# Optimization experiments

Hardware: AMD Instinct MI355X
Metric: run time of the kernel (lower is better)

## Reference

```python
import jax, jax.numpy as jnp
import numpy as np

B, S, D = 8, 4096, 512
BLOCK, LEFT, RIGHT = 64, 1, 1
FF = 2048
EPS = 1e-6


def setup_inputs() -> dict:
    key = jax.random.key(0)
    ks = jax.random.split(key, 16)
    sd = 1.0 / np.sqrt(D)
    sf = 1.0 / np.sqrt(FF)
    return {
        "x": jax.random.normal(ks[0], (B, S, D), jnp.float32),
        "Wq": jax.random.normal(ks[1], (D, D), jnp.float32) * sd,
        "bq": jnp.zeros((D,), jnp.float32),
        "Wk": jax.random.normal(ks[2], (D, D), jnp.float32) * sd,
        "bk": jnp.zeros((D,), jnp.float32),
        "Wv": jax.random.normal(ks[3], (D, D), jnp.float32) * sd,
        "bv": jnp.zeros((D,), jnp.float32),
        "W1": jax.random.normal(ks[4], (D, FF), jnp.float32) * sd,
        "b1": jnp.zeros((FF,), jnp.float32),
        "W2": jax.random.normal(ks[5], (FF, D), jnp.float32) * sf,
        "b2": jnp.zeros((D,), jnp.float32),
        "g1": jnp.ones((D,), jnp.float32),
        "be1": jnp.zeros((D,), jnp.float32),
        "g2": jnp.ones((D,), jnp.float32),
        "be2": jnp.zeros((D,), jnp.float32),
    }


def layernorm(x, g, b):
    m = jnp.mean(x, axis=-1, keepdims=True)
    v = jnp.mean(jnp.square(x - m), axis=-1, keepdims=True)
    return g * (x - m) * jax.lax.rsqrt(v + EPS) + b


def local_attention(x, Wq, bq, Wk, bk, Wv, bv):
    Bsz, Sl, Dm = x.shape
    nb = Sl // BLOCK          # number of blocks
    nw = LEFT + RIGHT + 1     # window (in blocks)
    q = (x @ Wq + bq).reshape(Bsz, nb, BLOCK, Dm)
    k = (x @ Wk + bk).reshape(Bsz, nb, BLOCK, Dm)
    v = (x @ Wv + bv).reshape(Bsz, nb, BLOCK, Dm)
    # pad block axis so every query block has LEFT/RIGHT neighbor blocks
    kp = jnp.pad(k, ((0, 0), (LEFT, RIGHT), (0, 0), (0, 0)))
    vp = jnp.pad(v, ((0, 0), (LEFT, RIGHT), (0, 0), (0, 0)))
    # gather windows: (B, nb, nw*BLOCK, D)
    k_win = jnp.stack([kp[:, j:j + nb] for j in range(nw)], axis=2).reshape(Bsz, nb, nw * BLOCK, Dm)
    v_win = jnp.stack([vp[:, j:j + nb] for j in range(nw)], axis=2).reshape(Bsz, nb, nw * BLOCK, Dm)
    # mask out-of-range (padded) blocks at sequence edges
    blk = jnp.arange(nb)[:, None] + jnp.arange(nw)[None, :] - LEFT  # (nb, nw)
    mask = ((blk >= 0) & (blk < nb))
    mask = jnp.repeat(mask, BLOCK, axis=1)  # (nb, nw*BLOCK)
    scores = jnp.einsum('bnqd,bnkd->bnqk', q, k_win) / jnp.sqrt(jnp.float32(Dm))
    scores = jnp.where(mask[None, :, None, :], scores, jnp.float32(-1e9))
    attn = jax.nn.softmax(scores, axis=-1)
    out = jnp.einsum('bnqk,bnkd->bnqd', attn, v_win)
    return out.reshape(Bsz, Sl, Dm)


def reference(x, Wq, bq, Wk, bk, Wv, bv, W1, b1, W2, b2, g1, be1, g2, be2):
    # inference mode: dropout is identity
    a = local_attention(x, Wq, bq, Wk, bk, Wv, bv)
    out1 = layernorm(x + a, g1, be1)
    ffn = jnp.maximum(out1 @ W1 + b1, 0.0) @ W2 + b2
    return layernorm(out1 + ffn, g2, be2)
```

## Files before the change

kernel.cpp:

```cpp
#include <hip/hip_runtime.h>


typedef __bf16 bf16;
typedef __bf16 bf16x8 __attribute__((ext_vector_type(8)));
typedef float  f32x4  __attribute__((ext_vector_type(4)));

#define DEV __device__ __forceinline__

#define BAR()  do { asm volatile("" ::: "memory"); __builtin_amdgcn_s_barrier(); asm volatile("" ::: "memory"); } while (0)
#define WAITV(n) asm volatile("s_waitcnt vmcnt(" #n ")" ::: "memory")
#define WAITL()  asm volatile("s_waitcnt lgkmcnt(0)" ::: "memory")

DEV void gload_lds16(const void* g, void* lds) {
  __builtin_amdgcn_global_load_lds(
      (const __attribute__((address_space(1))) void*)g,
      (__attribute__((address_space(3))) void*)lds, 16, 0, 0);
}

__global__ __launch_bounds__(256) void cast_to_bf16(const float* __restrict__ in,
                                                    bf16* __restrict__ out, int n8) {
  int i = blockIdx.x * 256 + threadIdx.x;
  if (i >= n8) return;
  float4 a0 = ((const float4*)in)[i * 2];
  float4 a1 = ((const float4*)in)[i * 2 + 1];
  bf16x8 o;
  o[0] = (bf16)a0.x; o[1] = (bf16)a0.y; o[2] = (bf16)a0.z; o[3] = (bf16)a0.w;
  o[4] = (bf16)a1.x; o[5] = (bf16)a1.y; o[6] = (bf16)a1.z; o[7] = (bf16)a1.w;
  ((bf16x8*)out)[i] = o;
}

__global__ __launch_bounds__(256) void transpose_cast(const float* __restrict__ W,
                                                      bf16* __restrict__ Wt, int K, int N) {
  __shared__ bf16 tile[64][66];
  const int n0 = blockIdx.x * 64, k0 = blockIdx.y * 64;
  const int t = threadIdx.x;
#pragma unroll
  for (int it = 0; it < 16; ++it) {
    int c = it * 256 + t;
    int kr = c >> 6, nc = c & 63;
    tile[nc][kr] = (bf16)W[(size_t)(k0 + kr) * N + n0 + nc];
  }
  __syncthreads();
#pragma unroll
  for (int it = 0; it < 2; ++it) {
    int c = it * 256 + t;
    int nr = c >> 3, kg = (c & 7) * 8;
    bf16x8 v;
#pragma unroll
    for (int e = 0; e < 8; ++e) v[e] = tile[nr][kg + e];
    *(bf16x8*)(Wt + (size_t)(n0 + nr) * K + k0 + kg) = v;
  }
}

__global__ __launch_bounds__(256) void concat_bias(const float* __restrict__ bq,
                                                   const float* __restrict__ bk,
                                                   const float* __restrict__ bv,
                                                   float* __restrict__ o) {
  int i = blockIdx.x * 256 + threadIdx.x;
  if (i < 512) o[i] = bq[i];
  else if (i < 1024) o[i] = bk[i - 512];
  else if (i < 1536) o[i] = bv[i - 1024];
}

template <int RELU, int F32OUT>
__global__ __launch_bounds__(512, 1)
void gemm256(const bf16* __restrict__ A, const bf16* __restrict__ Bt,
             const float* __restrict__ bias, void* __restrict__ Cout,
             int M, int N, int K) {
  __shared__ bf16x8 lds8[6144];
  char* const LB = (char*)lds8;
  const int tid = threadIdx.x;
  const int w = tid >> 6, l = tid & 63;
  const int lr = l & 15, lg = l >> 4;
  const int wm = w >> 2, wn = w & 3;

  const int nwg = gridDim.x * gridDim.y;
  const int bid = blockIdx.y * gridDim.x + blockIdx.x;
  const int cpx = nwg >> 3;
  const int swzb = (bid & 7) * cpx + (bid >> 3);
  const int m0 = (swzb & 127) * 256;
  const int n0 = (swzb >> 7) * 256;

  const int NT = K >> 5;

  const int srow = tid >> 2;
  const int scol = (((tid & 3) ^ (srow & 3)) << 3);
  const int swz = ((lg ^ (lr & 3)) << 4);

  f32x4 acc[8][4];
#pragma unroll
  for (int i = 0; i < 8; ++i)
#pragma unroll
    for (int j = 0; j < 4; ++j) acc[i][j] = f32x4{0.f, 0.f, 0.f, 0.f};

  auto stageA = [&](int t) {
    const bf16* g = A + (size_t)(m0 + srow) * K + t * 32 + scol;
    char* d = LB + (t % 3) * 32768 + tid * 16;
    gload_lds16(g, d);
    gload_lds16(g + (size_t)128 * K, d + 8192);
  };
  auto stageB = [&](int t) {
    const bf16* g = Bt + (size_t)(n0 + srow) * K + t * 32 + scol;
    char* d = LB + (t % 3) * 32768 + 16384 + tid * 16;
    gload_lds16(g, d);
    gload_lds16(g + (size_t)128 * K, d + 8192);
  };

  stageA(0); stageB(0);
  stageA(1); stageB(1);
  WAITV(4);
  BAR();

  for (int t = 0; t < NT; ++t) {
    const char* base = LB + (t % 3) * 32768;
    const char* pA = base + (wm << 13) + lr * 64 + swz;
    const char* pB = base + 16384 + (wn << 12) + lr * 64 + swz;
    if (t + 2 < NT) { stageA(t + 2); stageB(t + 2); }
    bf16x8 a0 = *(const bf16x8*)(pA);
    bf16x8 a1 = *(const bf16x8*)(pA + 1024);
    bf16x8 a2 = *(const bf16x8*)(pA + 2048);
    bf16x8 a3 = *(const bf16x8*)(pA + 3072);
    bf16x8 a4 = *(const bf16x8*)(pA + 4096);
    bf16x8 a5 = *(const bf16x8*)(pA + 5120);
    bf16x8 a6 = *(const bf16x8*)(pA + 6144);
    bf16x8 a7 = *(const bf16x8*)(pA + 7168);
    bf16x8 b0 = *(const bf16x8*)(pB);
    bf16x8 b1 = *(const bf16x8*)(pB + 1024);
    bf16x8 b2 = *(const bf16x8*)(pB + 2048);
    bf16x8 b3 = *(const bf16x8*)(pB + 3072);
    WAITL();
    __builtin_amdgcn_s_setprio(1);
    acc[0][0] = __builtin_amdgcn_mfma_f32_16x16x32_bf16(a0, b0, acc[0][0], 0, 0, 0);
    acc[0][1] = __builtin_amdgcn_mfma_f32_16x16x32_bf16(a0, b1, acc[0][1], 0, 0, 0);
    acc[0][2] = __builtin_amdgcn_mfma_f32_16x16x32_bf16(a0, b2, acc[0][2], 0, 0, 0);
    acc[0][3] = __builtin_amdgcn_mfma_f32_16x16x32_bf16(a0, b3, acc[0][3], 0, 0, 0);
    acc[1][0] = __builtin_amdgcn_mfma_f32_16x16x32_bf16(a1, b0, acc[1][0], 0, 0, 0);
    acc[1][1] = __builtin_amdgcn_mfma_f32_16x16x32_bf16(a1, b1, acc[1][1], 0, 0, 0);
    acc[1][2] = __builtin_amdgcn_mfma_f32_16x16x32_bf16(a1, b2, acc[1][2], 0, 0, 0);
    acc[1][3] = __builtin_amdgcn_mfma_f32_16x16x32_bf16(a1, b3, acc[1][3], 0, 0, 0);
    acc[2][0] = __builtin_amdgcn_mfma_f32_16x16x32_bf16(a2, b0, acc[2][0], 0, 0, 0);
    acc[2][1] = __builtin_amdgcn_mfma_f32_16x16x32_bf16(a2, b1, acc[2][1], 0, 0, 0);
    acc[2][2] = __builtin_amdgcn_mfma_f32_16x16x32_bf16(a2, b2, acc[2][2], 0, 0, 0);
    acc[2][3] = __builtin_amdgcn_mfma_f32_16x16x32_bf16(a2, b3, acc[2][3], 0, 0, 0);
    acc[3][0] = __builtin_amdgcn_mfma_f32_16x16x32_bf16(a3, b0, acc[3][0], 0, 0, 0);
    acc[3][1] = __builtin_amdgcn_mfma_f32_16x16x32_bf16(a3, b1, acc[3][1], 0, 0, 0);
    acc[3][2] = __builtin_amdgcn_mfma_f32_16x16x32_bf16(a3, b2, acc[3][2], 0, 0, 0);
    acc[3][3] = __builtin_amdgcn_mfma_f32_16x16x32_bf16(a3, b3, acc[3][3], 0, 0, 0);
    acc[4][0] = __builtin_amdgcn_mfma_f32_16x16x32_bf16(a4, b0, acc[4][0], 0, 0, 0);
    acc[4][1] = __builtin_amdgcn_mfma_f32_16x16x32_bf16(a4, b1, acc[4][1], 0, 0, 0);
    acc[4][2] = __builtin_amdgcn_mfma_f32_16x16x32_bf16(a4, b2, acc[4][2], 0, 0, 0);
    acc[4][3] = __builtin_amdgcn_mfma_f32_16x16x32_bf16(a4, b3, acc[4][3], 0, 0, 0);
    acc[5][0] = __builtin_amdgcn_mfma_f32_16x16x32_bf16(a5, b0, acc[5][0], 0, 0, 0);
    acc[5][1] = __builtin_amdgcn_mfma_f32_16x16x32_bf16(a5, b1, acc[5][1], 0, 0, 0);
    acc[5][2] = __builtin_amdgcn_mfma_f32_16x16x32_bf16(a5, b2, acc[5][2], 0, 0, 0);
    acc[5][3] = __builtin_amdgcn_mfma_f32_16x16x32_bf16(a5, b3, acc[5][3], 0, 0, 0);
    acc[6][0] = __builtin_amdgcn_mfma_f32_16x16x32_bf16(a6, b0, acc[6][0], 0, 0, 0);
    acc[6][1] = __builtin_amdgcn_mfma_f32_16x16x32_bf16(a6, b1, acc[6][1], 0, 0, 0);
    acc[6][2] = __builtin_amdgcn_mfma_f32_16x16x32_bf16(a6, b2, acc[6][2], 0, 0, 0);
    acc[6][3] = __builtin_amdgcn_mfma_f32_16x16x32_bf16(a6, b3, acc[6][3], 0, 0, 0);
    acc[7][0] = __builtin_amdgcn_mfma_f32_16x16x32_bf16(a7, b0, acc[7][0], 0, 0, 0);
    acc[7][1] = __builtin_amdgcn_mfma_f32_16x16x32_bf16(a7, b1, acc[7][1], 0, 0, 0);
    acc[7][2] = __builtin_amdgcn_mfma_f32_16x16x32_bf16(a7, b2, acc[7][2], 0, 0, 0);
    acc[7][3] = __builtin_amdgcn_mfma_f32_16x16x32_bf16(a7, b3, acc[7][3], 0, 0, 0);
    __builtin_amdgcn_s_setprio(0);
    if (t + 2 < NT) { WAITV(4); }
    else if (t + 2 == NT) { WAITV(0); }
    BAR();
  }

  if (!F32OUT) {
    bf16* cl = (bf16*)LB;
    bf16* Cb = (bf16*)Cout;
#pragma unroll
    for (int half = 0; half < 2; ++half) {
      if (wm == half) {
#pragma unroll
        for (int n = 0; n < 4; ++n) {
          const int col = (wn << 6) + (n << 4) + lr;
          const float bv = bias[n0 + col];
#pragma unroll
          for (int m = 0; m < 8; ++m)
#pragma unroll
            for (int rg = 0; rg < 4; ++rg) {
              const int row = (m << 4) + (lg << 2) + rg;
              float v = acc[m][n][rg] + bv;
              if (RELU) v = fmaxf(v, 0.f);
              cl[row * 256 + col] = (bf16)v;
            }
        }
      }
      __syncthreads();
#pragma unroll
      for (int it = 0; it < 8; ++it) {
        const int idx = it * 512 + tid;
        const int r = idx >> 5, ch = idx & 31;
        *(bf16x8*)(Cb + (size_t)(m0 + half * 128 + r) * N + n0 + (ch << 3)) =
            *(const bf16x8*)(cl + r * 256 + (ch << 3));
      }
      __syncthreads();
    }
  } else {
    float* Cf = (float*)Cout;
#pragma unroll
    for (int n = 0; n < 4; ++n) {
      const int col = n0 + (wn << 6) + (n << 4) + lr;
      const float bv = bias[col];
#pragma unroll
      for (int m = 0; m < 8; ++m)
#pragma unroll
        for (int rg = 0; rg < 4; ++rg) {
          const int row = m0 + (wm << 7) + (m << 4) + (lg << 2) + rg;
          float v = acc[m][n][rg] + bv;
          if (RELU) v = fmaxf(v, 0.f);
          Cf[(size_t)row * N + col] = v;
        }
    }
  }
}

__global__ __launch_bounds__(256) void transpose_v(const bf16* __restrict__ qkv,
                                                   bf16* __restrict__ vt) {
  __shared__ bf16 tile[64][66];
  const int s0 = blockIdx.x * 64, d0 = blockIdx.y * 64, b = blockIdx.z;
  const int t = threadIdx.x;
#pragma unroll
  for (int it = 0; it < 2; ++it) {
    int c = it * 256 + t;
    int r = c >> 3, g = (c & 7) * 8;
    bf16x8 v = *(const bf16x8*)(qkv + ((size_t)b * 4096 + s0 + r) * 1536 + 1024 + d0 + g);
#pragma unroll
    for (int e = 0; e < 8; ++e) tile[g + e][r] = v[e];
  }
  __syncthreads();
#pragma unroll
  for (int it = 0; it < 2; ++it) {
    int c = it * 256 + t;
    int dr = c >> 3, sg = (c & 7) * 8;
    bf16x8 v;
#pragma unroll
    for (int e = 0; e < 8; ++e) v[e] = tile[dr][sg + e];
    *(bf16x8*)(vt + ((size_t)b * 512 + d0 + dr) * 4096 + s0 + sg) = v;
  }
}

__global__ __launch_bounds__(512, 4)
void attn_local(const bf16* __restrict__ qkv, const bf16* __restrict__ vt,
                bf16* __restrict__ aout) {
  __shared__ bf16 P[4][16][200];
  __shared__ float xmx[4][2][16];
  __shared__ float xsm[4][2][16];
  const int qb = blockIdx.x, b = blockIdx.y;
  const int t = threadIdx.x, w = t >> 6, l = t & 63;
  const int rg = w & 3, h = w >> 2;
  const int lr = l & 15, lg = l >> 4;

  bool val[6];
#pragma unroll
  for (int n = 0; n < 6; ++n) {
    int gn = 6 * h + n;
    val[n] = ((unsigned)(qb - 1 + (gn >> 2)) < 64u);
  }

  const size_t qrow = (size_t)b * 4096 + qb * 64 + rg * 16;
  const bf16* qp = qkv + (qrow + lr) * 1536 + lg * 8;
  const bf16* kbase = qkv + ((long)b * 4096 + (long)(qb - 1) * 64) * 1536 + 512;

  f32x4 S[6];
#pragma unroll
  for (int n = 0; n < 6; ++n) S[n] = f32x4{0.f, 0.f, 0.f, 0.f};

  for (int kk = 0; kk < 16; ++kk) {
    bf16x8 aq = *(const bf16x8*)(qp + kk * 32);
#pragma unroll
    for (int n = 0; n < 6; ++n) {
      if (!val[n]) continue;
      const int gn = 6 * h + n;
      bf16x8 bk = *(const bf16x8*)(kbase + (size_t)(gn * 16 + lr) * 1536 + kk * 32 + lg * 8);
      S[n] = __builtin_amdgcn_mfma_f32_16x16x32_bf16(aq, bk, S[n], 0, 0, 0);
    }
  }

  const float scale = 0.044194173824159216f;
  float mx[4] = {-3e38f, -3e38f, -3e38f, -3e38f};
#pragma unroll
  for (int n = 0; n < 6; ++n) {
    if (!val[n]) continue;
#pragma unroll
    for (int i = 0; i < 4; ++i) mx[i] = fmaxf(mx[i], S[n][i]);
  }
#pragma unroll
  for (int i = 0; i < 4; ++i) {
    mx[i] = fmaxf(mx[i], __shfl_xor(mx[i], 1));
    mx[i] = fmaxf(mx[i], __shfl_xor(mx[i], 2));
    mx[i] = fmaxf(mx[i], __shfl_xor(mx[i], 4));
    mx[i] = fmaxf(mx[i], __shfl_xor(mx[i], 8));
  }
  if (lr == 0) {
#pragma unroll
    for (int i = 0; i < 4; ++i) xmx[rg][h][lg * 4 + i] = mx[i];
  }
  __syncthreads();
  float m4[4];
#pragma unroll
  for (int i = 0; i < 4; ++i) m4[i] = fmaxf(mx[i], xmx[rg][h ^ 1][lg * 4 + i]);

  float sm[4] = {0.f, 0.f, 0.f, 0.f};
#pragma unroll
  for (int n = 0; n < 6; ++n) {
    if (!val[n]) continue;
#pragma unroll
    for (int i = 0; i < 4; ++i) {
      float p = __expf((S[n][i] - m4[i]) * scale);
      S[n][i] = p;
      sm[i] += p;
    }
  }
#pragma unroll
  for (int i = 0; i < 4; ++i) {
    sm[i] += __shfl_xor(sm[i], 1);
    sm[i] += __shfl_xor(sm[i], 2);
    sm[i] += __shfl_xor(sm[i], 4);
    sm[i] += __shfl_xor(sm[i], 8);
  }
  if (lr == 0) {
#pragma unroll
    for (int i = 0; i < 4; ++i) xsm[rg][h][lg * 4 + i] = sm[i];
  }
  __syncthreads();
  float rinv[4];
#pragma unroll
  for (int i = 0; i < 4; ++i) rinv[i] = 1.f / (sm[i] + xsm[rg][h ^ 1][lg * 4 + i]);

#pragma unroll
  for (int n = 0; n < 6; ++n) {
    const int gn = 6 * h + n;
#pragma unroll
    for (int i = 0; i < 4; ++i)
      P[rg][lg * 4 + i][gn * 16 + lr] = val[n] ? (bf16)(S[n][i] * rinv[i]) : (bf16)0.f;
  }
  __syncthreads();

  f32x4 O[4][4];
#pragma unroll
  for (int rt = 0; rt < 4; ++rt)
#pragma unroll
    for (int dt = 0; dt < 4; ++dt) O[rt][dt] = f32x4{0.f, 0.f, 0.f, 0.f};

  const bf16* vtb = vt + ((long)b * 512 + w * 64) * 4096 + (long)(qb - 1) * 64;
#pragma unroll
  for (int ks = 0; ks < 6; ++ks) {
    if ((unsigned)(qb - 1 + (ks >> 1)) >= 64u) continue;
    bf16x8 vf[4];
#pragma unroll
    for (int dt = 0; dt < 4; ++dt)
      vf[dt] = *(const bf16x8*)(vtb + (size_t)(dt * 16 + lr) * 4096 + ks * 32 + lg * 8);
#pragma unroll
    for (int rt = 0; rt < 4; ++rt) {
      bf16x8 pa = *(const bf16x8*)&P[rt][lr][ks * 32 + lg * 8];
#pragma unroll
      for (int dt = 0; dt < 4; ++dt)
        O[rt][dt] = __builtin_amdgcn_mfma_f32_16x16x32_bf16(pa, vf[dt], O[rt][dt], 0, 0, 0);
    }
  }

  const size_t orow = (size_t)b * 4096 + qb * 64;
#pragma unroll
  for (int rt = 0; rt < 4; ++rt)
#pragma unroll
    for (int dt = 0; dt < 4; ++dt)
#pragma unroll
      for (int i = 0; i < 4; ++i)
        aout[(orow + rt * 16 + lg * 4 + i) * 512 + w * 64 + dt * 16 + lr] =
            (bf16)O[rt][dt][i];
}

__global__ __launch_bounds__(256) void ln_res1(const float* __restrict__ x,
                                               const bf16* __restrict__ a,
                                               const float* __restrict__ g,
                                               const float* __restrict__ be,
                                               bf16* __restrict__ out) {
  const int t = threadIdx.x, w = t >> 6, l = t & 63;
  const size_t row = (size_t)blockIdx.x * 4 + w;
  const float* xp = x + row * 512 + l * 8;
  float4 x0 = ((const float4*)xp)[0];
  float4 x1 = ((const float4*)xp)[1];
  bf16x8 av = *(const bf16x8*)(a + row * 512 + l * 8);
  float s[8] = {x0.x + (float)av[0], x0.y + (float)av[1], x0.z + (float)av[2], x0.w + (float)av[3],
                x1.x + (float)av[4], x1.y + (float)av[5], x1.z + (float)av[6], x1.w + (float)av[7]};
  float sum = 0.f;
#pragma unroll
  for (int i = 0; i < 8; ++i) sum += s[i];
#pragma unroll
  for (int m = 1; m <= 32; m <<= 1) sum += __shfl_xor(sum, m);
  const float mean = sum * (1.f / 512.f);
  float vs = 0.f;
#pragma unroll
  for (int i = 0; i < 8; ++i) { float d = s[i] - mean; vs += d * d; }
#pragma unroll
  for (int m = 1; m <= 32; m <<= 1) vs += __shfl_xor(vs, m);
  const float r = rsqrtf(vs * (1.f / 512.f) + 1e-6f);
  float4 g0 = ((const float4*)(g + l * 8))[0], g1 = ((const float4*)(g + l * 8))[1];
  float4 b0 = ((const float4*)(be + l * 8))[0], b1 = ((const float4*)(be + l * 8))[1];
  bf16x8 o;
  o[0] = (bf16)(g0.x * (s[0] - mean) * r + b0.x);
  o[1] = (bf16)(g0.y * (s[1] - mean) * r + b0.y);
  o[2] = (bf16)(g0.z * (s[2] - mean) * r + b0.z);
  o[3] = (bf16)(g0.w * (s[3] - mean) * r + b0.w);
  o[4] = (bf16)(g1.x * (s[4] - mean) * r + b1.x);
  o[5] = (bf16)(g1.y * (s[5] - mean) * r + b1.y);
  o[6] = (bf16)(g1.z * (s[6] - mean) * r + b1.z);
  o[7] = (bf16)(g1.w * (s[7] - mean) * r + b1.w);
  *(bf16x8*)(out + row * 512 + l * 8) = o;
}

__global__ __launch_bounds__(256) void ln_res2(const bf16* __restrict__ o1,
                                               float* __restrict__ y,
                                               const float* __restrict__ g,
                                               const float* __restrict__ be) {
  const int t = threadIdx.x, w = t >> 6, l = t & 63;
  const size_t row = (size_t)blockIdx.x * 4 + w;
  float* yp = y + row * 512 + l * 8;
  float4 y0 = ((const float4*)yp)[0];
  float4 y1 = ((const float4*)yp)[1];
  bf16x8 ov = *(const bf16x8*)(o1 + row * 512 + l * 8);
  float s[8] = {y0.x + (float)ov[0], y0.y + (float)ov[1], y0.z + (float)ov[2], y0.w + (float)ov[3],
                y1.x + (float)ov[4], y1.y + (float)ov[5], y1.z + (float)ov[6], y1.w + (float)ov[7]};
  float sum = 0.f;
#pragma unroll
  for (int i = 0; i < 8; ++i) sum += s[i];
#pragma unroll
  for (int m = 1; m <= 32; m <<= 1) sum += __shfl_xor(sum, m);
  const float mean = sum * (1.f / 512.f);
  float vs = 0.f;
#pragma unroll
  for (int i = 0; i < 8; ++i) { float d = s[i] - mean; vs += d * d; }
#pragma unroll
  for (int m = 1; m <= 32; m <<= 1) vs += __shfl_xor(vs, m);
  const float r = rsqrtf(vs * (1.f / 512.f) + 1e-6f);
  float4 g0 = ((const float4*)(g + l * 8))[0], g1 = ((const float4*)(g + l * 8))[1];
  float4 b0 = ((const float4*)(be + l * 8))[0], b1 = ((const float4*)(be + l * 8))[1];
  float4 r0, r1;
  r0.x = g0.x * (s[0] - mean) * r + b0.x;
  r0.y = g0.y * (s[1] - mean) * r + b0.y;
  r0.z = g0.z * (s[2] - mean) * r + b0.z;
  r0.w = g0.w * (s[3] - mean) * r + b0.w;
  r1.x = g1.x * (s[4] - mean) * r + b1.x;
  r1.y = g1.y * (s[5] - mean) * r + b1.y;
  r1.z = g1.z * (s[6] - mean) * r + b1.z;
  r1.w = g1.w * (s[7] - mean) * r + b1.w;
  ((float4*)yp)[0] = r0;
  ((float4*)yp)[1] = r1;
}

extern "C" void kernel_launch(void* const* d_in, const int* in_sizes, int n_in,
                              void* d_out, int out_size, void* d_ws, size_t ws_size,
                              hipStream_t stream) {
  const float* x   = (const float*)d_in[0];
  const float* Wq  = (const float*)d_in[1];
  const float* bq  = (const float*)d_in[2];
  const float* Wk  = (const float*)d_in[3];
  const float* bk  = (const float*)d_in[4];
  const float* Wv  = (const float*)d_in[5];
  const float* bv  = (const float*)d_in[6];
  const float* W1  = (const float*)d_in[7];
  const float* b1  = (const float*)d_in[8];
  const float* W2  = (const float*)d_in[9];
  const float* b2  = (const float*)d_in[10];
  const float* g1  = (const float*)d_in[11];
  const float* be1 = (const float*)d_in[12];
  const float* g2  = (const float*)d_in[13];
  const float* be2 = (const float*)d_in[14];
  float* out = (float*)d_out;

  char* ws = (char*)d_ws;
  bf16*  WqkvT = (bf16*)(ws + 0);
  bf16*  W1T   = (bf16*)(ws + 1572864);
  bf16*  W2T   = (bf16*)(ws + 3670016);
  float* bqkv  = (float*)(ws + 5767168);
  bf16*  xb    = (bf16*)(ws + 6291456);
  bf16*  out1  = (bf16*)(ws + 39845888);
  bf16*  qkv   = (bf16*)(ws + 73400320);
  bf16*  vtb   = (bf16*)(ws + 174063616);
  bf16*  a_    = xb;
  bf16*  h     = qkv;

  cast_to_bf16<<<8192, 256, 0, stream>>>(x, xb, 2097152);
  transpose_cast<<<dim3(8, 8), 256, 0, stream>>>(Wq, WqkvT, 512, 512);
  transpose_cast<<<dim3(8, 8), 256, 0, stream>>>(Wk, WqkvT + 262144, 512, 512);
  transpose_cast<<<dim3(8, 8), 256, 0, stream>>>(Wv, WqkvT + 524288, 512, 512);
  transpose_cast<<<dim3(32, 8), 256, 0, stream>>>(W1, W1T, 512, 2048);
  transpose_cast<<<dim3(8, 32), 256, 0, stream>>>(W2, W2T, 2048, 512);
  concat_bias<<<6, 256, 0, stream>>>(bq, bk, bv, bqkv);

  gemm256<0, 0><<<dim3(128, 6), 512, 0, stream>>>(xb, WqkvT, bqkv, qkv, 32768, 1536, 512);
  transpose_v<<<dim3(64, 8, 8), 256, 0, stream>>>(qkv, vtb);
  attn_local<<<dim3(64, 8), 512, 0, stream>>>(qkv, vtb, a_);
  ln_res1<<<8192, 256, 0, stream>>>(x, a_, g1, be1, out1);
  gemm256<1, 0><<<dim3(128, 8), 512, 0, stream>>>(out1, W1T, b1, h, 32768, 2048, 512);
  gemm256<0, 1><<<dim3(128, 2), 512, 0, stream>>>(h, W2T, b2, out, 32768, 512, 2048);
  ln_res2<<<8192, 256, 0, stream>>>(out1, out, g2, be2);
}
```

Measured before the change: 435.1 us.

## Switch GEMM to BK=64 double-buffered LDS pipeline with 8-way swizzle

The GEMM main loop moves from a 3-stage ring with K-step 32 to a 2-stage double buffer with K-step 64, using 128 KB of LDS and an XOR swizzle over 8 column groups. This halves the number of barriers and loop iterations and gives each wave more MFMA work per synchronisation. In exchange, only one tile is prefetched ahead, and the loop now waits for all outstanding loads (vmcnt 0) each iteration, which may expose global latency. The launch bound is also raised to ask for 2 blocks per CU, though 128 KB of LDS per block probably leaves room for only one.

```diff
diff --git a/kernel.cpp b/kernel.cpp
--- a/kernel.cpp
+++ b/kernel.cpp
@@ -8,8 +8,7 @@
 #define DEV __device__ __forceinline__
 
 #define BAR()  do { asm volatile("" ::: "memory"); __builtin_amdgcn_s_barrier(); asm volatile("" ::: "memory"); } while (0)
-#define WAITV(n) asm volatile("s_waitcnt vmcnt(" #n ")" ::: "memory")
-#define WAITL()  asm volatile("s_waitcnt lgkmcnt(0)" ::: "memory")
+#define WAITV0() asm volatile("s_waitcnt vmcnt(0)" ::: "memory")
 
 DEV void gload_lds16(const void* g, void* lds) {
   __builtin_amdgcn_global_load_lds(
@@ -63,11 +62,11 @@
 }
 
 template <int RELU, int F32OUT>
-__global__ __launch_bounds__(512, 1)
+__global__ __launch_bounds__(512, 2)
 void gemm256(const bf16* __restrict__ A, const bf16* __restrict__ Bt,
              const float* __restrict__ bias, void* __restrict__ Cout,
              int M, int N, int K) {
-  __shared__ bf16x8 lds8[6144];
+  __shared__ bf16x8 lds8[8192];
   char* const LB = (char*)lds8;
   const int tid = threadIdx.x;
   const int w = tid >> 6, l = tid & 63;
@@ -81,11 +80,18 @@
   const int m0 = (swzb & 127) * 256;
   const int n0 = (swzb >> 7) * 256;
 
-  const int NT = K >> 5;
-
-  const int srow = tid >> 2;
-  const int scol = (((tid & 3) ^ (srow & 3)) << 3);
-  const int swz = ((lg ^ (lr & 3)) << 4);
+  const int NT = K >> 6;
+
+  int srow[4], scol[4];
+#pragma unroll
+  for (int j = 0; j < 4; ++j) {
+    const int sg = tid + 512 * j;
+    srow[j] = sg >> 3;
+    scol[j] = (((sg & 7) ^ ((sg >> 3) & 7)) << 3);
+  }
+
+  const int swz0 = ((lg ^ (lr & 7)) << 4);
+  const int swz1 = (((4 | lg) ^ (lr & 7)) << 4);
 
   f32x4 acc[8][4];
 #pragma unroll
@@ -93,78 +99,41 @@
 #pragma unroll
     for (int j = 0; j < 4; ++j) acc[i][j] = f32x4{0.f, 0.f, 0.f, 0.f};
 
-  auto stageA = [&](int t) {
-    const bf16* g = A + (size_t)(m0 + srow) * K + t * 32 + scol;
-    char* d = LB + (t % 3) * 32768 + tid * 16;
-    gload_lds16(g, d);
-    gload_lds16(g + (size_t)128 * K, d + 8192);
+  auto stage = [&](int t) {
+    char* dA = LB + ((t & 1) << 16) + tid * 16;
+#pragma unroll
+    for (int j = 0; j < 4; ++j) {
+      gload_lds16(A + (size_t)(m0 + srow[j]) * K + t * 64 + scol[j], dA + j * 8192);
+      gload_lds16(Bt + (size_t)(n0 + srow[j]) * K + t * 64 + scol[j], dA + 32768 + j * 8192);
+    }
   };
-  auto stageB = [&](int t) {
-    const bf16* g = Bt + (size_t)(n0 + srow) * K + t * 32 + scol;
-    char* d = LB + (t % 3) * 32768 + 16384 + tid * 16;
-    gload_lds16(g, d);
-    gload_lds16(g + (size_t)128 * K, d + 8192);
-  };
-
-  stageA(0); stageB(0);
-  stageA(1); stageB(1);
-  WAITV(4);
+
+  stage(0);
+  WAITV0();
   BAR();
 
   for (int t = 0; t < NT; ++t) {
-    const char* base = LB + (t % 3) * 32768;
-    const char* pA = base + (wm << 13) + lr * 64 + swz;
-    const char* pB = base + 16384 + (wn << 12) + lr * 64 + swz;
-    if (t + 2 < NT) { stageA(t + 2); stageB(t + 2); }
-    bf16x8 a0 = *(const bf16x8*)(pA);
-    bf16x8 a1 = *(const bf16x8*)(pA + 1024);
-    bf16x8 a2 = *(const bf16x8*)(pA + 2048);
-    bf16x8 a3 = *(const bf16x8*)(pA + 3072);
-    bf16x8 a4 = *(const bf16x8*)(pA + 4096);
-    bf16x8 a5 = *(const bf16x8*)(pA + 5120);
-    bf16x8 a6 = *(const bf16x8*)(pA + 6144);
-    bf16x8 a7 = *(const bf16x8*)(pA + 7168);
-    bf16x8 b0 = *(const bf16x8*)(pB);
-    bf16x8 b1 = *(const bf16x8*)(pB + 1024);
-    bf16x8 b2 = *(const bf16x8*)(pB + 2048);
-    bf16x8 b3 = *(const bf16x8*)(pB + 3072);
-    WAITL();
-    __builtin_amdgcn_s_setprio(1);
-    acc[0][0] = __builtin_amdgcn_mfma_f32_16x16x32_bf16(a0, b0, acc[0][0], 0, 0, 0);
-    acc[0][1] = __builtin_amdgcn_mfma_f32_16x16x32_bf16(a0, b1, acc[0][1], 0, 0, 0);
-    acc[0][2] = __builtin_amdgcn_mfma_f32_16x16x32_bf16(a0, b2, acc[0][2], 0, 0, 0);
-    acc[0][3] = __builtin_amdgcn_mfma_f32_16x16x32_bf16(a0, b3, acc[0][3], 0, 0, 0);
-    acc[1][0] = __builtin_amdgcn_mfma_f32_16x16x32_bf16(a1, b0, acc[1][0], 0, 0, 0);
-    acc[1][1] = __builtin_amdgcn_mfma_f32_16x16x32_bf16(a1, b1, acc[1][1], 0, 0, 0);
-    acc[1][2] = __builtin_amdgcn_mfma_f32_16x16x32_bf16(a1, b2, acc[1][2], 0, 0, 0);
-    acc[1][3] = __builtin_amdgcn_mfma_f32_16x16x32_bf16(a1, b3, acc[1][3], 0, 0, 0);
-    acc[2][0] = __builtin_amdgcn_mfma_f32_16x16x32_bf16(a2, b0, acc[2][0], 0, 0, 0);
-    acc[2][1] = __builtin_amdgcn_mfma_f32_16x16x32_bf16(a2, b1, acc[2][1], 0, 0, 0);
-    acc[2][2] = __builtin_amdgcn_mfma_f32_16x16x32_bf16(a2, b2, acc[2][2], 0, 0, 0);
-    acc[2][3] = __builtin_amdgcn_mfma_f32_16x16x32_bf16(a2, b3, acc[2][3], 0, 0, 0);
-    acc[3][0] = __builtin_amdgcn_mfma_f32_16x16x32_bf16(a3, b0, acc[3][0], 0, 0, 0);
-    acc[3][1] = __builtin_amdgcn_mfma_f32_16x16x32_bf16(a3, b1, acc[3][1], 0, 0, 0);
-    acc[3][2] = __builtin_amdgcn_mfma_f32_16x16x32_bf16(a3, b2, acc[3][2], 0, 0, 0);
-    acc[3][3] = __builtin_amdgcn_mfma_f32_16x16x32_bf16(a3, b3, acc[3][3], 0, 0, 0);
-    acc[4][0] = __builtin_amdgcn_mfma_f32_16x16x32_bf16(a4, b0, acc[4][0], 0, 0, 0);
-    acc[4][1] = __builtin_amdgcn_mfma_f32_16x16x32_bf16(a4, b1, acc[4][1], 0, 0, 0);
-    acc[4][2] = __builtin_amdgcn_mfma_f32_16x16x32_bf16(a4, b2, acc[4][2], 0, 0, 0);
-    acc[4][3] = __builtin_amdgcn_mfma_f32_16x16x32_bf16(a4, b3, acc[4][3], 0, 0, 0);
-    acc[5][0] = __builtin_amdgcn_mfma_f32_16x16x32_bf16(a5, b0, acc[5][0], 0, 0, 0);
-    acc[5][1] = __builtin_amdgcn_mfma_f32_16x16x32_bf16(a5, b1, acc[5][1], 0, 0, 0);
-    acc[5][2] = __builtin_amdgcn_mfma_f32_16x16x32_bf16(a5, b2, acc[5][2], 0, 0, 0);
-    acc[5][3] = __builtin_amdgcn_mfma_f32_16x16x32_bf16(a5, b3, acc[5][3], 0, 0, 0);
-    acc[6][0] = __builtin_amdgcn_mfma_f32_16x16x32_bf16(a6, b0, acc[6][0], 0, 0, 0);
-    acc[6][1] = __builtin_amdgcn_mfma_f32_16x16x32_bf16(a6, b1, acc[6][1], 0, 0, 0);
-    acc[6][2] = __builtin_amdgcn_mfma_f32_16x16x32_bf16(a6, b2, acc[6][2], 0, 0, 0);
-    acc[6][3] = __builtin_amdgcn_mfma_f32_16x16x32_bf16(a6, b3, acc[6][3], 0, 0, 0);
-    acc[7][0] = __builtin_amdgcn_mfma_f32_16x16x32_bf16(a7, b0, acc[7][0], 0, 0, 0);
-    acc[7][1] = __builtin_amdgcn_mfma_f32_16x16x32_bf16(a7, b1, acc[7][1], 0, 0, 0);
-    acc[7][2] = __builtin_amdgcn_mfma_f32_16x16x32_bf16(a7, b2, acc[7][2], 0, 0, 0);
-    acc[7][3] = __builtin_amdgcn_mfma_f32_16x16x32_bf16(a7, b3, acc[7][3], 0, 0, 0);
-    __builtin_amdgcn_s_setprio(0);
-    if (t + 2 < NT) { WAITV(4); }
-    else if (t + 2 == NT) { WAITV(0); }
+    if (t + 1 < NT) stage(t + 1);
+    const char* base = LB + ((t & 1) << 16);
+    const char* pA = base + (wm << 14) + (lr << 7);
+    const char* pB = base + 32768 + (wn << 13) + (lr << 7);
+    bf16x8 bv_[4][2];
+#pragma unroll
+    for (int n = 0; n < 4; ++n) {
+      bv_[n][0] = *(const bf16x8*)(pB + n * 2048 + swz0);
+      bv_[n][1] = *(const bf16x8*)(pB + n * 2048 + swz1);
+    }
+#pragma unroll
+    for (int i = 0; i < 8; ++i) {
+      bf16x8 a0 = *(const bf16x8*)(pA + i * 2048 + swz0);
+      bf16x8 a1 = *(const bf16x8*)(pA + i * 2048 + swz1);
+#pragma unroll
+      for (int n = 0; n < 4; ++n) {
+        acc[i][n] = __builtin_amdgcn_mfma_f32_16x16x32_bf16(a0, bv_[n][0], acc[i][n], 0, 0, 0);
+        acc[i][n] = __builtin_amdgcn_mfma_f32_16x16x32_bf16(a1, bv_[n][1], acc[i][n], 0, 0, 0);
+      }
+    }
+    WAITV0();
     BAR();
   }
 
```

Result: faster. 413.3 us (-5.0%).
